# Performance work log

Measured on AMD Instinct MI355X. Metric: run time of the kernel, lower is better.

## Reference

```python
import jax, jax.numpy as jnp
import numpy as np
from jax import lax

B, F, T, H = 32, 1024, 512, 64
ENC_SIZES = [2*F+1, 1387, 726, H]      # linear interp 2049 -> 64, depth 3
DEC_SIZES = [F+H+1, 1067, 1046, F]     # linear interp 1089 -> 1024, depth 3


def _mlp(ws, bs, x):
    # fully connected stack, ReLU between layers, no final activation
    n = len(ws)
    for i in range(n):
        x = x @ ws[i] + bs[i]
        if i < n - 1:
            x = jax.nn.relu(x)
    return x


def setup_inputs() -> dict:
    key = jax.random.key(0)
    ks = jax.random.split(key, 8)
    d = {"x": jax.random.normal(ks[0], (B, F, T), dtype=jnp.float32)}
    for i, (fin, fout) in enumerate(zip(ENC_SIZES[:-1], ENC_SIZES[1:])):
        d[f"ew{i}"] = jax.random.normal(ks[1+i], (fin, fout), jnp.float32) / np.sqrt(fin)
        d[f"eb{i}"] = jnp.zeros((fout,), jnp.float32)
    for i, (fin, fout) in enumerate(zip(DEC_SIZES[:-1], DEC_SIZES[1:])):
        d[f"dw{i}"] = jax.random.normal(ks[4+i], (fin, fout), jnp.float32) / np.sqrt(fin)
        d[f"db{i}"] = jnp.zeros((fout,), jnp.float32)
    return d


def reference(x, ew0, eb0, ew1, eb1, ew2, eb2, dw0, db0, dw1, db1, dw2, db2):
    enc_w, enc_b = (ew0, ew1, ew2), (eb0, eb1, eb2)
    dec_w, dec_b = (dw0, dw1, dw2), (db0, db1, db2)
    b = x.shape[0]
    xs = jnp.moveaxis(x, 2, 0)                       # [T, B, F]
    ts = (jnp.arange(T, dtype=x.dtype) / T)          # [T]

    # ---- encode: prev_stft feedback recurrence ----
    def enc_step(prev_stft, inp):
        curr, tval = inp
        tcol = jnp.full((b, 1), tval, dtype=x.dtype)
        comb = jnp.concatenate([prev_stft, curr, tcol], axis=1)  # [B, 2F+1]
        h = _mlp(enc_w, enc_b, comb)                             # [B, H]
        return curr, h

    _, hs = lax.scan(enc_step, jnp.zeros((b, F), x.dtype), (xs, ts))
    # flatten(-2) then view(B,H,T) round-trips, so keep [T,B,H]; tanh applied after flatten
    hiddens = jnp.tanh(hs)                           # [T, B, H]

    # ---- decode: prev_stft = decoder output recurrence ----
    def dec_step(prev_stft, inp):
        h_t, tval = inp
        tcol = jnp.full((b, 1), tval, dtype=x.dtype)
        comb = jnp.concatenate([h_t, prev_stft, tcol], axis=1)   # [B, H+F+1]
        out = _mlp(dec_w, dec_b, comb)                           # [B, F]
        return out, out

    _, ys = lax.scan(dec_step, jnp.zeros((b, F), x.dtype), (hiddens, ts))
    return jnp.transpose(ys, (1, 2, 0))              # [B, F, T]
```

## Files before the change

kernel.cpp:

```cpp
#include <hip/hip_runtime.h>
#include <hip/hip_bf16.h>
#include <hip/hip_fp16.h>


typedef _Float16 f16x8 __attribute__((ext_vector_type(8)));
typedef float f32x4 __attribute__((ext_vector_type(4)));
typedef unsigned short u16;
typedef unsigned int u32;
typedef unsigned long long u64;

#define MFMA(a, b, c) __builtin_amdgcn_mfma_f32_16x16x32_f16((a), (b), (c), 0, 0, 0)

__device__ __forceinline__ float h2f(u16 u) { __half h; __builtin_memcpy(&h, &u, 2); return __half2float(h); }
__device__ __forceinline__ u16 f2h(float f) { __half h = __float2half(f); u16 u; __builtin_memcpy(&u, &h, 2); return u; }

__device__ __forceinline__ void st_act4(u32* p, u32 v) {
  __hip_atomic_store(p, v, __ATOMIC_RELAXED, __HIP_MEMORY_SCOPE_AGENT);
}
__device__ __forceinline__ f16x8 ld_act16(const u16* p) {
  u64 lo = __hip_atomic_load((const u64*)p, __ATOMIC_RELAXED, __HIP_MEMORY_SCOPE_AGENT);
  u64 hi = __hip_atomic_load((const u64*)(p + 4), __ATOMIC_RELAXED, __HIP_MEMORY_SCOPE_AGENT);
  union { u64 q[2]; f16x8 v; } u;
  u.q[0] = lo; u.q[1] = hi;
  return u.v;
}

__device__ __forceinline__ void pack_body(const float* __restrict__ W, int ldw, int row0,
                                          int Kr, int Nr, u16* __restrict__ out, int Np,
                                          int id, int total) {
  if (id >= total) return;
  int kq = id / Np, n = id % Np;
  union { u16 v[8]; uint4 q; } un;
#pragma unroll
  for (int j = 0; j < 8; ++j) {
    int k = kq * 8 + j;
    float f = (k < Kr && n < Nr) ? W[(size_t)(row0 + k) * ldw + n] : 0.f;
    un.v[j] = f2h(f);
  }
  *(uint4*)(out + (size_t)id * 8) = un.q;
}

__global__ __launch_bounds__(256) void prep_kernel(
    const float* __restrict__ ew0, const float* __restrict__ ew1, const float* __restrict__ ew2,
    const float* __restrict__ dw0, const float* __restrict__ dw1, const float* __restrict__ dw2,
    const float* __restrict__ db2,
    u16* We0p, u16* We1p, u16* We2p, u16* Wh0p, u16* Wd0p, u16* Wd1p, u16* Wd2p,
    u16* xT, float* c2x, int* flags, u16* acts) {
  const int b = blockIdx.x, tid = threadIdx.x;
  if (b < 1408) {
    pack_body(ew0, 1387, 0, 2048, 1387, We0p, 1408, b * 256 + tid, 256 * 1408);
  } else if (b < 1936) {
    pack_body(ew1, 726, 0, 1387, 726, We1p, 768, (b - 1408) * 256 + tid, 176 * 768);
  } else if (b < 1960) {
    pack_body(ew2, 64, 0, 726, 64, We2p, 64, (b - 1936) * 256 + tid, 96 * 64);
  } else if (b < 1996) {
    pack_body(dw0, 1067, 0, 64, 1067, Wh0p, 1152, (b - 1960) * 256 + tid, 8 * 1152);
  } else if (b < 2644) {
    pack_body(dw0, 1067, 64, 1024, 1067, Wd0p, 1152, (b - 1996) * 256 + tid, 144 * 1152);
  } else if (b < 3292) {
    pack_body(dw1, 1046, 0, 1067, 1046, Wd1p, 1152, (b - 2644) * 256 + tid, 144 * 1152);
  } else if (b < 3940) {
    pack_body(dw2, 1024, 0, 1046, 1024, Wd2p, 1152, (b - 3292) * 256 + tid, 144 * 1152);
  } else if (b < 4068) {
    int i = (b - 3940) * 256 + tid;
    if (i < 32768) xT[i] = 0;
  } else if (b < 4073) {
    int n = (b - 4068) * 256 + tid;
    if (n < 1152) {
      float s = 0.f;
      if (n < 1067) {
        for (int k = 0; k < 1024; ++k) s += db2[k] * dw0[(size_t)(64 + k) * 1067 + n];
      }
      c2x[n] = s;
    }
  } else if (b < 4082) {
    int i = (b - 4073) * 256 + tid;
    if (i < 2144) flags[i] = 0;
  } else {
    int i = (b - 4082) * 256 + tid;
    if (i < 9216) { uint4 z = {}; *(uint4*)(acts + (size_t)i * 8) = z; }
  }
}

__global__ __launch_bounds__(256) void transpose_kernel(const float* __restrict__ x, u16* __restrict__ xT) {
  __shared__ float tile[64][65];
  int b = blockIdx.z, f0 = blockIdx.x * 64, t0 = blockIdx.y * 64;
  const float* xp = x + (size_t)b * (1024 * 512);
  for (int rep = 0; rep < 16; ++rep) {
    int e = rep * 256 + threadIdx.x;
    int fi = e >> 6, tj = e & 63;
    tile[fi][tj] = xp[(size_t)(f0 + fi) * 512 + t0 + tj];
  }
  __syncthreads();
  for (int rep = 0; rep < 16; ++rep) {
    int e = rep * 256 + threadIdx.x;
    int tj = e >> 6, fi = e & 63;
    xT[(size_t)((t0 + tj + 1) * 32 + b) * 1024 + f0 + fi] = f2h(tile[fi][tj]);
  }
}

__global__ __launch_bounds__(256) void cvt_a_kernel(const float* __restrict__ src, u16* __restrict__ dst) {
  int i = blockIdx.x * 256 + threadIdx.x;
  int r = i >> 10;
  dst[i] = f2h(r < 1046 ? src[i] : 0.f);
}

template <int TWOSRC, int ACT, int T1, int T2, int PACKO>
__global__ __launch_bounds__(256) void gemm_kernel(
    const u16* __restrict__ A, int lda,
    const u16* __restrict__ Wp, int Np,
    const float* __restrict__ bias, int nb,
    const float* __restrict__ wt1, int nw1,
    const float* __restrict__ wt2, int nw2,
    u16* __restrict__ out, int ldo, int Kp) {
  __shared__ u16 As[128][72];
  __shared__ u16 Bs[8 * 64 * 8];
  const int tid = threadIdx.x;
  const int bx = blockIdx.x, by = blockIdx.y;
  const int m0 = by * 128, n0 = bx * 64;
  const int l = tid & 63, wv = tid >> 6, lm = l & 15, lg = l >> 4;
  f32x4 acc[2][4] = {};
  for (int k0 = 0; k0 < Kp; k0 += 64) {
#pragma unroll
    for (int c = 0; c < 4; ++c) {
      int idx = c * 256 + tid;
      int row = idx >> 3, seg = idx & 7;
      int kk = k0 + seg * 8;
      const u16* ap;
      if (TWOSRC) {
        int half = (kk >= 1024) ? 1 : 0;
        ap = A + (size_t)(m0 + row + half * 32) * lda + (kk - half * 1024);
      } else {
        ap = A + (size_t)(m0 + row) * lda + kk;
      }
      *(uint4*)&As[row][seg * 8] = *(const uint4*)ap;
    }
#pragma unroll
    for (int c = 0; c < 2; ++c) {
      int idx = c * 256 + tid;
      int e0 = idx * 8;
      int kq = e0 >> 9, inner = e0 & 511;
      const u16* gp = Wp + (size_t)((k0 >> 3) + kq) * (Np * 8) + n0 * 8 + inner;
      *(uint4*)(Bs + e0) = *(const uint4*)gp;
    }
    __syncthreads();
#pragma unroll
    for (int ks = 0; ks < 2; ++ks) {
      f16x8 af0 = *(const f16x8*)&As[wv * 32 + lm][ks * 32 + lg * 8];
      f16x8 af1 = *(const f16x8*)&As[wv * 32 + 16 + lm][ks * 32 + lg * 8];
#pragma unroll
      for (int nf = 0; nf < 4; ++nf) {
        f16x8 bfr = *(const f16x8*)(Bs + ((ks * 4 + lg) * 64 + nf * 16 + lm) * 8);
        acc[0][nf] = MFMA(af0, bfr, acc[0][nf]);
        acc[1][nf] = MFMA(af1, bfr, acc[1][nf]);
      }
    }
    __syncthreads();
  }
#pragma unroll
  for (int mr = 0; mr < 2; ++mr) {
    int rb = m0 + wv * 32 + mr * 16;
    int tt = rb >> 5;
#pragma unroll
    for (int nf = 0; nf < 4; ++nf) {
      int col = n0 + nf * 16 + lm;
      float bv = (col < nb) ? bias[col] : 0.f;
      if (T1) bv += (float)tt * (1.f / 512.f) * ((col < nw1) ? wt1[col] : 0.f);
      if (T2) bv += ((tt > 0) ? 1.f : 0.f) * ((col < nw2) ? wt2[col] : 0.f);
#pragma unroll
      for (int v = 0; v < 4; ++v) {
        float xv = acc[mr][nf][v] + bv;
        if (ACT == 1) xv = fmaxf(xv, 0.f);
        if (ACT == 2) xv = tanhf(xv);
        if (PACKO) {
          int r = rb + lg * 4 + v;
          out[((size_t)(r >> 3) * Np + col) * 8 + (r & 7)] = f2h(xv);
        } else {
          out[(size_t)(rb + lg * 4 + v) * ldo + col] = f2h(xv);
        }
      }
    }
  }
}

#define NWG 67

__device__ __forceinline__ void gbar(int* flags, int bid, int tid, int gen) {
  asm volatile("s_waitcnt vmcnt(0)" ::: "memory");
  __syncthreads();
  if (tid == 0)
    __hip_atomic_store(flags + bid * 32, gen, __ATOMIC_RELAXED, __HIP_MEMORY_SCOPE_AGENT);
  if (tid < NWG) {
    while (__hip_atomic_load(flags + tid * 32, __ATOMIC_RELAXED, __HIP_MEMORY_SCOPE_AGENT) < gen)
      __builtin_amdgcn_s_sleep(1);
  }
  __syncthreads();
}

__device__ __forceinline__ void dec_mm(const u16* __restrict__ in, const u16* wl,
                                       float (*red)[512], int tid, int lm, int lg, int wv,
                                       int e0, float& s0, float& s1) {
  const int kq0 = wv * 36;
  f32x4 acc0 = {}, acc1 = {};
#pragma unroll
  for (int ks = 0; ks < 9; ++ks) {
    int kq = kq0 + ks * 4 + lg;
    const u16* pa = in + kq * 256 + lm * 8;
    f16x8 a0f = ld_act16(pa);
    f16x8 a1f = ld_act16(pa + 128);
    f16x8 bf = *(const f16x8*)(wl + ((size_t)kq * 16 + lm) * 8);
    acc0 = MFMA(a0f, bf, acc0);
    acc1 = MFMA(a1f, bf, acc1);
  }
#pragma unroll
  for (int v = 0; v < 4; ++v) {
    red[wv][(lg * 4 + v) * 16 + lm] = acc0[v];
    red[wv][(16 + lg * 4 + v) * 16 + lm] = acc1[v];
  }
  __syncthreads();
  s0 = red[0][e0] + red[1][e0] + red[2][e0] + red[3][e0];
  s1 = red[0][e0 + 1] + red[1][e0 + 1] + red[2][e0 + 1] + red[3][e0 + 1];
}

__global__ __launch_bounds__(256, 1) void decoder_kernel(
    const u16* __restrict__ W1p, const u16* __restrict__ Mp,
    const u16* __restrict__ hpart, const float* __restrict__ db1,
    u16* a0, u16* a1, u16* __restrict__ a1buf, int* flags) {
  __shared__ __align__(16) u16 wlds[2 * 2304 * 8];
  __shared__ float red[4][512];
  const int tid = threadIdx.x, bid = blockIdx.x;
  const int l = tid & 63, wv = tid >> 6, lm = l & 15, lg = l >> 4;
  const int n0 = bid * 16;
  for (int i = tid; i < 2 * 2304; i += 256) {
    int layer = i / 2304, rem = i % 2304, kq = rem >> 4, c = rem & 15;
    const u16* base = (layer == 0) ? W1p : Mp;
    *(uint4*)(wlds + (size_t)i * 8) = *(const uint4*)(base + ((size_t)kq * 1152 + n0 + c) * 8);
  }
  const int e0 = tid * 2, row = e0 >> 4, c0 = e0 & 15, na = n0 + c0;
  u32* a0slot = (u32*)(a0 + (((size_t)(na >> 3) * 32 + row) * 8 + (na & 7)));
  u32* a1slot = (u32*)(a1 + (((size_t)(na >> 3) * 32 + row) * 8 + (na & 7)));
  const float bv0 = (na < 1046) ? db1[na] : 0.f;
  const float bv1 = (na + 1 < 1046) ? db1[na + 1] : 0.f;
  int gen = 0;
  __syncthreads();
  {
    u32 pk = *(const u32*)(hpart + row * 1152 + na);
    float s0 = fmaxf(h2f((u16)(pk & 0xffff)), 0.f);
    float s1 = fmaxf(h2f((u16)(pk >> 16)), 0.f);
    st_act4(a0slot, (u32)f2h(s0) | ((u32)f2h(s1) << 16));
  }
  gbar(flags, bid, tid, ++gen);
#pragma unroll 1
  for (int t = 0; t < 512; ++t) {
    u32 hpk = 0;
    if (t < 511) hpk = *(const u32*)(hpart + (size_t)(t + 1) * 36864 + row * 1152 + na);
    float s0, s1;
    dec_mm(a0, wlds, red, tid, lm, lg, wv, e0, s0, s1);
    s0 = fmaxf(s0 + bv0, 0.f);
    s1 = fmaxf(s1 + bv1, 0.f);
    u32 opk = (u32)f2h(s0) | ((u32)f2h(s1) << 16);
    if (t == 511) {
      *(u32*)(a1buf + ((size_t)(t * 32 + row) * 1088 + na)) = opk;
      break;
    }
    st_act4(a1slot, opk);
    gbar(flags, bid, tid, ++gen);
    *(u32*)(a1buf + ((size_t)(t * 32 + row) * 1088 + na)) = opk;
    dec_mm(a1, wlds + 2304 * 8, red, tid, lm, lg, wv, e0, s0, s1);
    s0 = fmaxf(s0 + h2f((u16)(hpk & 0xffff)), 0.f);
    s1 = fmaxf(s1 + h2f((u16)(hpk >> 16)), 0.f);
    st_act4(a0slot, (u32)f2h(s0) | ((u32)f2h(s1) << 16));
    gbar(flags, bid, tid, ++gen);
  }
}

__global__ __launch_bounds__(256) void finalize_kernel(const u16* __restrict__ ytmp,
                                                       float* __restrict__ dout) {
  __shared__ float tile[64][65];
  int b = blockIdx.z, n0 = blockIdx.x * 64, t0 = blockIdx.y * 64;
  for (int rep = 0; rep < 16; ++rep) {
    int e = rep * 256 + threadIdx.x;
    int tt = e >> 6, nn = e & 63;
    tile[tt][nn] = h2f(ytmp[(size_t)((t0 + tt) * 32 + b) * 1024 + n0 + nn]);
  }
  __syncthreads();
  for (int rep = 0; rep < 16; ++rep) {
    int e = rep * 256 + threadIdx.x;
    int nn = e >> 6, tt = e & 63;
    dout[((size_t)b * 1024 + n0 + nn) * 512 + t0 + tt] = tile[tt][nn];
  }
}

extern "C" void kernel_launch(void* const* d_in, const int* in_sizes, int n_in,
                              void* d_out, int out_size, void* d_ws, size_t ws_size,
                              hipStream_t stream) {
  (void)in_sizes; (void)n_in; (void)out_size; (void)ws_size;
  const float* x   = (const float*)d_in[0];
  const float* ew0 = (const float*)d_in[1];
  const float* eb0 = (const float*)d_in[2];
  const float* ew1 = (const float*)d_in[3];
  const float* eb1 = (const float*)d_in[4];
  const float* ew2 = (const float*)d_in[5];
  const float* eb2 = (const float*)d_in[6];
  const float* dw0 = (const float*)d_in[7];
  const float* db0 = (const float*)d_in[8];
  const float* dw1 = (const float*)d_in[9];
  const float* db1 = (const float*)d_in[10];
  const float* dw2 = (const float*)d_in[11];
  const float* db2 = (const float*)d_in[12];

  char* ws = (char*)d_ws;
  u16* xT    = (u16*)(ws + 0);
  u16* ytmp  = (u16*)(ws + 0);
  u16* act2  = (u16*)(ws + 33619968ull);
  u16* A16   = (u16*)(ws + 33619968ull);
  u16* Mp    = (u16*)(ws + 33619968ull + 2359296ull);
  u16* hid   = (u16*)(ws + 58785792ull);
  u16* hpart = (u16*)(ws + 60882944ull);
  u16* We0p  = (u16*)(ws + 98631680ull);
  u16* We1p  = (u16*)(ws + 104398848ull);
  u16* We2p  = (u16*)(ws + 106561536ull);
  u16* Wh0p  = (u16*)(ws + 106659840ull);
  u16* Wd0p  = (u16*)(ws + 106807296ull);
  u16* Wd1p  = (u16*)(ws + 109461504ull);
  u16* Wd2p  = (u16*)(ws + 112115712ull);
  float* c2x = (float*)(ws + 114769920ull);
  u16* a0    = (u16*)(ws + 114774528ull);
  u16* a1    = (u16*)(ws + 114848256ull);
  int* flags = (int*)(ws + 114921984ull);

  u16* act1  = (u16*)d_out;
  u16* a1buf = (u16*)d_out;
  float* dout = (float*)d_out;

  prep_kernel<<<dim3(4118), dim3(256), 0, stream>>>(
      ew0, ew1, ew2, dw0, dw1, dw2, db2,
      We0p, We1p, We2p, Wh0p, Wd0p, Wd1p, Wd2p, xT, c2x, flags, a0);

  transpose_kernel<<<dim3(16, 8, 32), dim3(256), 0, stream>>>(x, xT);

  gemm_kernel<1, 1, 1, 0, 0><<<dim3(22, 128), dim3(256), 0, stream>>>(
      xT, 1024, We0p, 1408, eb0, 1387, ew0 + (size_t)2048 * 1387, 1387, nullptr, 0, act1, 1408, 2048);
  gemm_kernel<0, 1, 0, 0, 0><<<dim3(12, 128), dim3(256), 0, stream>>>(
      act1, 1408, We1p, 768, eb1, 726, nullptr, 0, nullptr, 0, act2, 768, 1408);
  gemm_kernel<0, 2, 0, 0, 0><<<dim3(1, 128), dim3(256), 0, stream>>>(
      act2, 768, We2p, 64, eb2, 64, nullptr, 0, nullptr, 0, hid, 64, 768);
  gemm_kernel<0, 0, 1, 1, 0><<<dim3(18, 128), dim3(256), 0, stream>>>(
      hid, 64, Wh0p, 1152, db0, 1067, dw0 + (size_t)1088 * 1067, 1067, c2x, 1152, hpart, 1152, 64);

  cvt_a_kernel<<<dim3(4608), dim3(256), 0, stream>>>(dw2, A16);
  gemm_kernel<0, 0, 0, 0, 1><<<dim3(18, 9), dim3(256), 0, stream>>>(
      A16, 1024, Wd0p, 1152, nullptr, 0, nullptr, 0, nullptr, 0, Mp, 0, 1024);

  decoder_kernel<<<dim3(NWG), dim3(256), 0, stream>>>(Wd1p, Mp, hpart, db1, a0, a1, a1buf, flags);

  gemm_kernel<0, 0, 0, 0, 0><<<dim3(16, 128), dim3(256), 0, stream>>>(
      a1buf, 1088, Wd2p, 1152, db2, 1024, nullptr, 0, nullptr, 0, ytmp, 1024, 1088);
  finalize_kernel<<<dim3(16, 8, 32), dim3(256), 0, stream>>>(ytmp, dout);
}
```

Baseline: 3.600 ms.

## Overlap final decoder GEMM with recurrence using consumer workgroups in the persistent kernel

Adds 64 extra consumer workgroups to the persistent decoder kernel. They poll the producer barrier flags and compute the last decoder layer (a1buf x W2 + bias) in chunks of 2048 rows as the recurrence produces each chunk. This replaces the separate GEMM launch that ran after the recurrence finished. Each consumer covers four 128x64 tiles per chunk. The a1buf stores become atomic agent-scope stores issued before the barrier so consumers can see them. The risks are contention with the latency-bound recurrence for bandwidth and compute, and a polling loop with a bounded iteration cutoff that could read incomplete data if it times out.

```diff
diff --git a/kernel.cpp b/kernel.cpp
--- a/kernel.cpp
+++ b/kernel.cpp
@@ -184,6 +184,7 @@
 }
 
 #define NWG 67
+#define NCONS 64
 
 __device__ __forceinline__ void gbar(int* flags, int bid, int tid, int gen) {
   asm volatile("s_waitcnt vmcnt(0)" ::: "memory");
@@ -225,11 +226,78 @@
 __global__ __launch_bounds__(256, 1) void decoder_kernel(
     const u16* __restrict__ W1p, const u16* __restrict__ Mp,
     const u16* __restrict__ hpart, const float* __restrict__ db1,
-    u16* a0, u16* a1, u16* __restrict__ a1buf, int* flags) {
+    u16* a0, u16* a1, u16* __restrict__ a1buf, int* flags,
+    const u16* __restrict__ W2p, const float* __restrict__ db2, u16* __restrict__ ytmp) {
   __shared__ __align__(16) u16 wlds[2 * 2304 * 8];
   __shared__ float red[4][512];
   const int tid = threadIdx.x, bid = blockIdx.x;
   const int l = tid & 63, wv = tid >> 6, lm = l & 15, lg = l >> 4;
+
+  if (bid >= NWG) {
+    const int cid = bid - NWG;
+    u16* As = wlds;
+    u16* Bs = wlds + 128 * 72;
+#pragma unroll 1
+    for (int e = 0; e < 8; ++e) {
+      const int target = 128 * e + 128;
+      if (tid < NWG) {
+        int it = 0;
+        while (__hip_atomic_load(flags + tid * 32, __ATOMIC_RELAXED, __HIP_MEMORY_SCOPE_AGENT) < target) {
+          __builtin_amdgcn_s_sleep(64);
+          if (++it >= 4096) break;
+        }
+      }
+      __syncthreads();
+#pragma unroll 1
+      for (int j = 0; j < 4; ++j) {
+        const int tile = cid * 4 + j;
+        const int m0 = e * 2048 + (tile >> 4) * 128;
+        const int n0 = (tile & 15) * 64;
+        f32x4 acc[2][4] = {};
+#pragma unroll 1
+        for (int k0 = 0; k0 < 1088; k0 += 64) {
+#pragma unroll
+          for (int c = 0; c < 4; ++c) {
+            int idx = c * 256 + tid, row = idx >> 3, seg = idx & 7;
+            f16x8 v = ld_act16(a1buf + (size_t)(m0 + row) * 1088 + k0 + seg * 8);
+            *(f16x8*)&As[row * 72 + seg * 8] = v;
+          }
+#pragma unroll
+          for (int c = 0; c < 2; ++c) {
+            int idx = c * 256 + tid, e2 = idx * 8, kq = e2 >> 9, inner = e2 & 511;
+            *(uint4*)(Bs + e2) = *(const uint4*)(W2p + (size_t)((k0 >> 3) + kq) * (1152 * 8) + n0 * 8 + inner);
+          }
+          __syncthreads();
+#pragma unroll
+          for (int ks = 0; ks < 2; ++ks) {
+            f16x8 af0 = *(const f16x8*)&As[(wv * 32 + lm) * 72 + ks * 32 + lg * 8];
+            f16x8 af1 = *(const f16x8*)&As[(wv * 32 + 16 + lm) * 72 + ks * 32 + lg * 8];
+#pragma unroll
+            for (int nf = 0; nf < 4; ++nf) {
+              f16x8 bfr = *(const f16x8*)(Bs + ((ks * 4 + lg) * 64 + nf * 16 + lm) * 8);
+              acc[0][nf] = MFMA(af0, bfr, acc[0][nf]);
+              acc[1][nf] = MFMA(af1, bfr, acc[1][nf]);
+            }
+          }
+          __syncthreads();
+        }
+#pragma unroll
+        for (int mr = 0; mr < 2; ++mr) {
+          int rb = m0 + wv * 32 + mr * 16;
+#pragma unroll
+          for (int nf = 0; nf < 4; ++nf) {
+            int col = n0 + nf * 16 + lm;
+            float bv = db2[col];
+#pragma unroll
+            for (int v = 0; v < 4; ++v)
+              ytmp[(size_t)(rb + lg * 4 + v) * 1024 + col] = f2h(acc[mr][nf][v] + bv);
+          }
+        }
+      }
+    }
+    return;
+  }
+
   const int n0 = bid * 16;
   for (int i = tid; i < 2 * 2304; i += 256) {
     int layer = i / 2304, rem = i % 2304, kq = rem >> 4, c = rem & 15;
@@ -259,13 +327,10 @@
     s0 = fmaxf(s0 + bv0, 0.f);
     s1 = fmaxf(s1 + bv1, 0.f);
     u32 opk = (u32)f2h(s0) | ((u32)f2h(s1) << 16);
-    if (t == 511) {
-      *(u32*)(a1buf + ((size_t)(t * 32 + row) * 1088 + na)) = opk;
-      break;
-    }
     st_act4(a1slot, opk);
+    st_act4((u32*)(a1buf + ((size_t)(t * 32 + row) * 1088 + na)), opk);
     gbar(flags, bid, tid, ++gen);
-    *(u32*)(a1buf + ((size_t)(t * 32 + row) * 1088 + na)) = opk;
+    if (t == 511) break;
     dec_mm(a1, wlds + 2304 * 8, red, tid, lm, lg, wv, e0, s0, s1);
     s0 = fmaxf(s0 + h2f((u16)(hpk & 0xffff)), 0.f);
     s1 = fmaxf(s1 + h2f((u16)(hpk >> 16)), 0.f);
@@ -352,9 +417,8 @@
   gemm_kernel<0, 0, 0, 0, 1><<<dim3(18, 9), dim3(256), 0, stream>>>(
       A16, 1024, Wd0p, 1152, nullptr, 0, nullptr, 0, nullptr, 0, Mp, 0, 1024);
 
-  decoder_kernel<<<dim3(NWG), dim3(256), 0, stream>>>(Wd1p, Mp, hpart, db1, a0, a1, a1buf, flags);
-
-  gemm_kernel<0, 0, 0, 0, 0><<<dim3(16, 128), dim3(256), 0, stream>>>(
-      a1buf, 1088, Wd2p, 1152, db2, 1024, nullptr, 0, nullptr, 0, ytmp, 1024, 1088);
+  decoder_kernel<<<dim3(NWG + NCONS), dim3(256), 0, stream>>>(
+      Wd1p, Mp, hpart, db1, a0, a1, a1buf, flags, Wd2p, db2, ytmp);
+
   finalize_kernel<<<dim3(16, 8, 32), dim3(256), 0, stream>>>(ytmp, dout);
 }
```

Measured after the change: 3.645 ms. Within noise of the previous version (+1.2%).

## Replace decoder global barriers with per-producer dataflow flag waits

Applied to the files above, without the earlier changes.

Drops the all-workgroup barrier between decoder layers. Each wave now spins only on the flags of the producer workgroups whose activation slices it reads, then loads those activations. It also issues all activation loads before the MFMA chain so their latency overlaps. The aim is to cut barrier latency on the serial 512-step recurrence. The trade-off is that without a full barrier, a fast workgroup may overwrite a ping-pong buffer that a slower workgroup has not finished reading, so correctness relies on the dependency chain implicitly bounding skew.

```diff
diff --git a/kernel.cpp b/kernel.cpp
--- a/kernel.cpp
+++ b/kernel.cpp
@@ -185,32 +185,40 @@
 
 #define NWG 67
 
-__device__ __forceinline__ void gbar(int* flags, int bid, int tid, int gen) {
-  asm volatile("s_waitcnt vmcnt(0)" ::: "memory");
-  __syncthreads();
-  if (tid == 0)
-    __hip_atomic_store(flags + bid * 32, gen, __ATOMIC_RELAXED, __HIP_MEMORY_SCOPE_AGENT);
-  if (tid < NWG) {
-    while (__hip_atomic_load(flags + tid * 32, __ATOMIC_RELAXED, __HIP_MEMORY_SCOPE_AGENT) < gen)
-      __builtin_amdgcn_s_sleep(1);
-  }
-  __syncthreads();
-}
-
-__device__ __forceinline__ void dec_mm(const u16* __restrict__ in, const u16* wl,
-                                       float (*red)[512], int tid, int lm, int lg, int wv,
-                                       int e0, float& s0, float& s1) {
+__device__ __forceinline__ void dec_mm_df(const u16* __restrict__ in, const u16* wl,
+                                          const int* flags, int gen_in,
+                                          float (*red)[512], int lm, int lg, int wv,
+                                          int e0, float& s0, float& s1) {
   const int kq0 = wv * 36;
-  f32x4 acc0 = {}, acc1 = {};
+  for (;;) {
+    int mn = 0x7fffffff;
+#pragma unroll
+    for (int ks = 0; ks < 9; ++ks) {
+      int prod = (kq0 + ks * 4 + lg) >> 1;
+      if (prod < NWG) {
+        int f = __hip_atomic_load(flags + prod * 32, __ATOMIC_RELAXED, __HIP_MEMORY_SCOPE_AGENT);
+        mn = f < mn ? f : mn;
+      }
+    }
+    if (mn >= gen_in) break;
+    __builtin_amdgcn_s_sleep(1);
+  }
+  asm volatile("" ::: "memory");
+  f16x8 av0[9], av1[9];
 #pragma unroll
   for (int ks = 0; ks < 9; ++ks) {
     int kq = kq0 + ks * 4 + lg;
     const u16* pa = in + kq * 256 + lm * 8;
-    f16x8 a0f = ld_act16(pa);
-    f16x8 a1f = ld_act16(pa + 128);
+    av0[ks] = ld_act16(pa);
+    av1[ks] = ld_act16(pa + 128);
+  }
+  f32x4 acc0 = {}, acc1 = {};
+#pragma unroll
+  for (int ks = 0; ks < 9; ++ks) {
+    int kq = kq0 + ks * 4 + lg;
     f16x8 bf = *(const f16x8*)(wl + ((size_t)kq * 16 + lm) * 8);
-    acc0 = MFMA(a0f, bf, acc0);
-    acc1 = MFMA(a1f, bf, acc1);
+    acc0 = MFMA(av0[ks], bf, acc0);
+    acc1 = MFMA(av1[ks], bf, acc1);
   }
 #pragma unroll
   for (int v = 0; v < 4; ++v) {
@@ -225,7 +233,7 @@
 __global__ __launch_bounds__(256, 1) void decoder_kernel(
     const u16* __restrict__ W1p, const u16* __restrict__ Mp,
     const u16* __restrict__ hpart, const float* __restrict__ db1,
-    u16* a0, u16* a1, u16* __restrict__ a1buf, int* flags) {
+    u16* actp0, u16* actp1, u16* __restrict__ a1buf, int* flags) {
   __shared__ __align__(16) u16 wlds[2 * 2304 * 8];
   __shared__ float red[4][512];
   const int tid = threadIdx.x, bid = blockIdx.x;
@@ -237,40 +245,46 @@
     *(uint4*)(wlds + (size_t)i * 8) = *(const uint4*)(base + ((size_t)kq * 1152 + n0 + c) * 8);
   }
   const int e0 = tid * 2, row = e0 >> 4, c0 = e0 & 15, na = n0 + c0;
-  u32* a0slot = (u32*)(a0 + (((size_t)(na >> 3) * 32 + row) * 8 + (na & 7)));
-  u32* a1slot = (u32*)(a1 + (((size_t)(na >> 3) * 32 + row) * 8 + (na & 7)));
+  const size_t slotoff = ((size_t)(na >> 3) * 32 + row) * 8 + (na & 7);
+  u32* slot0 = (u32*)(actp0 + slotoff);
+  u32* slot1 = (u32*)(actp1 + slotoff);
   const float bv0 = (na < 1046) ? db1[na] : 0.f;
   const float bv1 = (na + 1 < 1046) ? db1[na + 1] : 0.f;
-  int gen = 0;
-  __syncthreads();
+  int* myflag = flags + bid * 32;
   {
     u32 pk = *(const u32*)(hpart + row * 1152 + na);
     float s0 = fmaxf(h2f((u16)(pk & 0xffff)), 0.f);
     float s1 = fmaxf(h2f((u16)(pk >> 16)), 0.f);
-    st_act4(a0slot, (u32)f2h(s0) | ((u32)f2h(s1) << 16));
-  }
-  gbar(flags, bid, tid, ++gen);
+    st_act4(slot1, (u32)f2h(s0) | ((u32)f2h(s1) << 16));
+  }
+  asm volatile("s_waitcnt vmcnt(0)" ::: "memory");
+  __syncthreads();
+  if (tid == 0) __hip_atomic_store(myflag, 1, __ATOMIC_RELAXED, __HIP_MEMORY_SCOPE_AGENT);
+  int gen = 1;
 #pragma unroll 1
   for (int t = 0; t < 512; ++t) {
     u32 hpk = 0;
     if (t < 511) hpk = *(const u32*)(hpart + (size_t)(t + 1) * 36864 + row * 1152 + na);
     float s0, s1;
-    dec_mm(a0, wlds, red, tid, lm, lg, wv, e0, s0, s1);
+    dec_mm_df(actp1, wlds, flags, gen, red, lm, lg, wv, e0, s0, s1);
     s0 = fmaxf(s0 + bv0, 0.f);
     s1 = fmaxf(s1 + bv1, 0.f);
     u32 opk = (u32)f2h(s0) | ((u32)f2h(s1) << 16);
-    if (t == 511) {
-      *(u32*)(a1buf + ((size_t)(t * 32 + row) * 1088 + na)) = opk;
-      break;
-    }
-    st_act4(a1slot, opk);
-    gbar(flags, bid, tid, ++gen);
     *(u32*)(a1buf + ((size_t)(t * 32 + row) * 1088 + na)) = opk;
-    dec_mm(a1, wlds + 2304 * 8, red, tid, lm, lg, wv, e0, s0, s1);
+    if (t == 511) break;
+    st_act4(slot0, opk);
+    asm volatile("s_waitcnt vmcnt(0)" ::: "memory");
+    __syncthreads();
+    ++gen;
+    if (tid == 0) __hip_atomic_store(myflag, gen, __ATOMIC_RELAXED, __HIP_MEMORY_SCOPE_AGENT);
+    dec_mm_df(actp0, wlds + 2304 * 8, flags, gen, red, lm, lg, wv, e0, s0, s1);
     s0 = fmaxf(s0 + h2f((u16)(hpk & 0xffff)), 0.f);
     s1 = fmaxf(s1 + h2f((u16)(hpk >> 16)), 0.f);
-    st_act4(a0slot, (u32)f2h(s0) | ((u32)f2h(s1) << 16));
-    gbar(flags, bid, tid, ++gen);
+    st_act4(slot1, (u32)f2h(s0) | ((u32)f2h(s1) << 16));
+    asm volatile("s_waitcnt vmcnt(0)" ::: "memory");
+    __syncthreads();
+    ++gen;
+    if (tid == 0) __hip_atomic_store(myflag, gen, __ATOMIC_RELAXED, __HIP_MEMORY_SCOPE_AGENT);
   }
 }
 
@@ -325,8 +339,8 @@
   u16* Wd1p  = (u16*)(ws + 109461504ull);
   u16* Wd2p  = (u16*)(ws + 112115712ull);
   float* c2x = (float*)(ws + 114769920ull);
-  u16* a0    = (u16*)(ws + 114774528ull);
-  u16* a1    = (u16*)(ws + 114848256ull);
+  u16* actp0 = (u16*)(ws + 114774528ull);
+  u16* actp1 = (u16*)(ws + 114848256ull);
   int* flags = (int*)(ws + 114921984ull);
 
   u16* act1  = (u16*)d_out;
@@ -335,7 +349,7 @@
 
   prep_kernel<<<dim3(4118), dim3(256), 0, stream>>>(
       ew0, ew1, ew2, dw0, dw1, dw2, db2,
-      We0p, We1p, We2p, Wh0p, Wd0p, Wd1p, Wd2p, xT, c2x, flags, a0);
+      We0p, We1p, We2p, Wh0p, Wd0p, Wd1p, Wd2p, xT, c2x, flags, actp0);
 
   transpose_kernel<<<dim3(16, 8, 32), dim3(256), 0, stream>>>(x, xT);
 
@@ -352,7 +366,7 @@
   gemm_kernel<0, 0, 0, 0, 1><<<dim3(18, 9), dim3(256), 0, stream>>>(
       A16, 1024, Wd0p, 1152, nullptr, 0, nullptr, 0, nullptr, 0, Mp, 0, 1024);
 
-  decoder_kernel<<<dim3(NWG), dim3(256), 0, stream>>>(Wd1p, Mp, hpart, db1, a0, a1, a1buf, flags);
+  decoder_kernel<<<dim3(NWG), dim3(256), 0, stream>>>(Wd1p, Mp, hpart, db1, actp0, actp1, a1buf, flags);
 
   gemm_kernel<0, 0, 0, 0, 0><<<dim3(16, 128), dim3(256), 0, stream>>>(
       a1buf, 1088, Wd2p, 1152, db2, 1024, nullptr, 0, nullptr, 0, ytmp, 1024, 1088);
```

Result: slower. 5.180 ms (+43.9%).
